# Kernel optimization log

Hardware: AMD Instinct MI355X
Metric: run time of the kernel (lower is better)

## Reference

```python
import jax, jax.numpy as jnp
import numpy as np

N = 50000


def gcn_conv(x, edge_index, W, b):
    # x: [N, F_in], edge_index: [2, E] (row=source j, col=target i)
    n = x.shape[0]
    loops = jnp.arange(n, dtype=edge_index.dtype)
    row = jnp.concatenate([edge_index[0], loops])
    col = jnp.concatenate([edge_index[1], loops])
    # linear transform first (PyG GCNConv)
    xw = x @ W  # [N, F_out]
    # symmetric normalization deg^{-1/2}[row] * deg^{-1/2}[col]
    deg = jax.ops.segment_sum(jnp.ones_like(col, dtype=xw.dtype), col, num_segments=n)
    dis = jnp.where(deg > 0, jax.lax.rsqrt(jnp.maximum(deg, 1e-12)), 0.0)
    norm = dis[row] * dis[col]  # [E+N]
    # gather-scale-scatter: sum_j norm_ij * (W x_j)
    msgs = xw[row] * norm[:, None]
    out = jax.ops.segment_sum(msgs, col, num_segments=n)
    return out + b


def setup_inputs() -> dict:
    key = jax.random.key(0)
    k1, k2, k3, k4, k5 = jax.random.split(key, 5)
    in_dim, hidden_dim, out_dim = 128, 128, 64
    x = jax.random.normal(k1, (N, in_dim), dtype=jnp.float32)
    edge_index = jax.random.randint(k2, (2, 800000), 0, N, dtype=jnp.int64)
    s1 = 1.0 / np.sqrt(in_dim)
    s2 = 1.0 / np.sqrt(hidden_dim)
    W1 = jax.random.uniform(k3, (in_dim, hidden_dim), jnp.float32, -s1, s1)
    b1 = jnp.zeros((hidden_dim,), jnp.float32)
    W2 = jax.random.uniform(k4, (hidden_dim, out_dim), jnp.float32, -s2, s2)
    b2 = jnp.zeros((out_dim,), jnp.float32)
    return {"x": x, "edge_index": edge_index, "W1": W1, "b1": b1, "W2": W2, "b2": b2}


def reference(x, edge_index, W1, b1, W2, b2):
    h = gcn_conv(x, edge_index, W1, b1)
    h = jax.nn.relu(h)
    # dropout(p=0.5, training=False) -> identity (inference reference)
    out = gcn_conv(h, edge_index, W2, b2)
    return out
```

## Files before the change

kernel.cpp:

```cpp
#include <hip/hip_runtime.h>
#include <hip/hip_fp16.h>


typedef _Float16 half8 __attribute__((ext_vector_type(8)));
typedef float floatx4 __attribute__((ext_vector_type(4)));

__global__ void k_count(const int* __restrict__ col, int* __restrict__ deg,
                        int* __restrict__ rank, int E) {
    int e = blockIdx.x * blockDim.x + threadIdx.x;
    if (e < E) rank[e] = atomicAdd(&deg[col[e]], 1);
}

__global__ __launch_bounds__(1024) void k_scan_local(const int* __restrict__ deg,
                                                     int* __restrict__ rowptr,
                                                     int* __restrict__ bsum,
                                                     float* __restrict__ dis, int n) {
    __shared__ int s[1024];
    int b = blockIdx.x, tid = threadIdx.x;
    int i = b * 1024 + tid;
    int v = (i < n) ? deg[i] : 0;
    if (i < n) dis[i] = rsqrtf((float)v + 1.0f);
    s[tid] = v;
    __syncthreads();
    for (int off = 1; off < 1024; off <<= 1) {
        int t = (tid >= off) ? s[tid - off] : 0;
        __syncthreads();
        s[tid] += t;
        __syncthreads();
    }
    if (i < n) rowptr[i + 1] = s[tid];
    if (tid == 1023) bsum[b] = s[1023];
    if (b == 0 && tid == 0) rowptr[0] = 0;
}

__global__ __launch_bounds__(256) void k_scan_fix(int* __restrict__ rowptr,
                                                  const int* __restrict__ bsum, int n) {
    __shared__ int red[256];
    int b = blockIdx.x, tid = threadIdx.x;
    int partial = 0;
    for (int j = tid; j < b; j += 256) partial += bsum[j];
    red[tid] = partial;
    __syncthreads();
    for (int off = 128; off > 0; off >>= 1) {
        if (tid < off) red[tid] += red[tid + off];
        __syncthreads();
    }
    int offv = red[0];
    if (offv == 0) return;
#pragma unroll
    for (int r = 0; r < 4; ++r) {
        int i = b * 1024 + r * 256 + tid;
        if (i < n) rowptr[i + 1] += offv;
    }
}

__global__ void k_fill(const int* __restrict__ row, const int* __restrict__ col,
                       const int* __restrict__ rowptr, const int* __restrict__ rank,
                       int* __restrict__ csr, int E) {
    int e = blockIdx.x * blockDim.x + threadIdx.x;
    if (e < E) csr[rowptr[col[e]] + rank[e]] = row[e];
}

template <int N, typename AT>
__global__ __launch_bounds__(256) void k_gemm_mfma(const AT* __restrict__ X,
                                                   const float* __restrict__ W,
                                                   const float* __restrict__ scale,
                                                   __half* __restrict__ Y, int M) {
    __shared__ __align__(16) __half2 wt[N * 64];
    int tid = threadIdx.x;
    for (int i = tid; i < N * 64; i += 256) {
        int nn = i & (N - 1);
        int k2 = i / N;
        float w0 = W[(size_t)(2 * k2) * N + nn];
        float w1 = W[(size_t)(2 * k2 + 1) * N + nn];
        wt[nn * 64 + ((k2 >> 2) ^ (nn & 15)) * 4 + (k2 & 3)] = __floats2half2_rn(w0, w1);
    }
    __syncthreads();
    int wid = tid >> 6, lane = tid & 63;
    int col = lane & 15, quad = lane >> 4;
    int m_a = blockIdx.x * 64 + wid * 16 + col;
    bool a_ok = m_a < M;
    constexpr int NT = N / 16;
    floatx4 acc[NT] = {};
#pragma unroll
    for (int ks = 0; ks < 4; ++ks) {
        int k = ks * 32 + quad * 8;
        half8 af;
        if constexpr (sizeof(AT) == 4) {
            floatx4 a0 = {0.f, 0.f, 0.f, 0.f}, a1 = {0.f, 0.f, 0.f, 0.f};
            if (a_ok) {
                a0 = *(const floatx4*)&X[(size_t)m_a * 128 + k];
                a1 = *(const floatx4*)&X[(size_t)m_a * 128 + k + 4];
            }
            af = half8{(_Float16)a0[0], (_Float16)a0[1], (_Float16)a0[2], (_Float16)a0[3],
                       (_Float16)a1[0], (_Float16)a1[1], (_Float16)a1[2], (_Float16)a1[3]};
        } else {
            half8 t = {};
            if (a_ok) t = *(const half8*)(const void*)&X[(size_t)m_a * 128 + k];
            af = t;
        }
        int kblk = ks * 4 + quad;
#pragma unroll
        for (int nt = 0; nt < NT; ++nt) {
            int nn = nt * 16 + col;
            half8 bf = *(const half8*)(const void*)&wt[nn * 64 + (kblk ^ (nn & 15)) * 4];
            acc[nt] = __builtin_amdgcn_mfma_f32_16x16x32_f16(af, bf, acc[nt], 0, 0, 0);
        }
    }
    int mbase = blockIdx.x * 64 + wid * 16 + quad * 4;
    float s[4];
#pragma unroll
    for (int r = 0; r < 4; ++r) s[r] = (mbase + r < M) ? scale[mbase + r] : 0.f;
#pragma unroll
    for (int nt = 0; nt < NT; ++nt) {
#pragma unroll
        for (int r = 0; r < 4; ++r) {
            if (mbase + r < M)
                Y[(size_t)(mbase + r) * N + nt * 16 + col] = __float2half(acc[nt][r] * s[r]);
        }
    }
}

__global__ __launch_bounds__(256) void k_agg128(const __half* __restrict__ xw,
                                                const float* __restrict__ dis,
                                                const int* __restrict__ rowptr,
                                                const int* __restrict__ csr,
                                                const float* __restrict__ bias,
                                                __half* __restrict__ out, int n) {
    int tid = threadIdx.x;
    int lane = tid & 63;
    int q = lane >> 4, li = lane & 15;
    int qbase = lane & 48;
    int node = blockIdx.x * 16 + ((tid >> 6) << 2) + q;
    bool ok = node < n;
    float di = 0.f;
    int beg = 0, end = 0;
    if (ok) {
        di = dis[node];
        beg = rowptr[node];
        end = rowptr[node + 1];
    }
    int dg = end - beg;
    int m1 = max(dg, __shfl(dg, lane ^ 16));
    int mx = max(m1, __shfl(m1, lane ^ 32));
    const half8* rows = (const half8*)xw;
    float acc[8] = {};
    if (ok) {
        half8 sf = rows[(size_t)node * 16 + li];
#pragma unroll
        for (int f = 0; f < 8; ++f) acc[f] = (float)sf[f];
    }
    for (int i = 0; i < mx; i += 8) {
        int e = beg + i + (li & 7);
        int myidx = (e < end) ? csr[e] : 0;
        half8 v[8];
#pragma unroll
        for (int j = 0; j < 8; ++j) {
            int s = __shfl(myidx, qbase + j);
            v[j] = rows[(size_t)s * 16 + li];
        }
#pragma unroll
        for (int j = 0; j < 8; ++j) {
            if (beg + i + j < end) {
#pragma unroll
                for (int f = 0; f < 8; ++f) acc[f] += (float)v[j][f];
            }
        }
    }
    if (ok) {
        floatx4 b0 = *(const floatx4*)&bias[li * 8];
        floatx4 b1 = *(const floatx4*)&bias[li * 8 + 4];
        half8 o;
#pragma unroll
        for (int f = 0; f < 4; ++f) o[f] = (_Float16)fmaxf(acc[f] * di + b0[f], 0.f);
#pragma unroll
        for (int f = 0; f < 4; ++f) o[4 + f] = (_Float16)fmaxf(acc[4 + f] * di + b1[f], 0.f);
        ((half8*)out)[(size_t)node * 16 + li] = o;
    }
}

__global__ __launch_bounds__(256) void k_agg64(const __half* __restrict__ xw,
                                               const float* __restrict__ dis,
                                               const int* __restrict__ rowptr,
                                               const int* __restrict__ csr,
                                               const float* __restrict__ bias,
                                               float* __restrict__ out, int n) {
    int tid = threadIdx.x;
    int lane = tid & 63;
    int o8 = lane >> 3, li = lane & 7;
    int obase = lane & 56;
    int node = blockIdx.x * 32 + ((tid >> 6) << 3) + o8;
    bool ok = node < n;
    float di = 0.f;
    int beg = 0, end = 0;
    if (ok) {
        di = dis[node];
        beg = rowptr[node];
        end = rowptr[node + 1];
    }
    int dg = end - beg;
    int m1 = max(dg, __shfl(dg, lane ^ 8));
    int m2 = max(m1, __shfl(m1, lane ^ 16));
    int mx = max(m2, __shfl(m2, lane ^ 32));
    const half8* rows = (const half8*)xw;
    float acc[8] = {};
    if (ok) {
        half8 sf = rows[(size_t)node * 8 + li];
#pragma unroll
        for (int f = 0; f < 8; ++f) acc[f] = (float)sf[f];
    }
    for (int i = 0; i < mx; i += 8) {
        int e = beg + i + li;
        int myidx = (e < end) ? csr[e] : 0;
        half8 v[8];
#pragma unroll
        for (int j = 0; j < 8; ++j) {
            int s = __shfl(myidx, obase + j);
            v[j] = rows[(size_t)s * 8 + li];
        }
#pragma unroll
        for (int j = 0; j < 8; ++j) {
            if (beg + i + j < end) {
#pragma unroll
                for (int f = 0; f < 8; ++f) acc[f] += (float)v[j][f];
            }
        }
    }
    if (ok) {
        floatx4 b0 = *(const floatx4*)&bias[li * 8];
        floatx4 b1 = *(const floatx4*)&bias[li * 8 + 4];
        floatx4 o0, o1;
#pragma unroll
        for (int f = 0; f < 4; ++f) o0[f] = acc[f] * di + b0[f];
#pragma unroll
        for (int f = 0; f < 4; ++f) o1[f] = acc[4 + f] * di + b1[f];
        *(floatx4*)&out[(size_t)node * 64 + li * 8] = o0;
        *(floatx4*)&out[(size_t)node * 64 + li * 8 + 4] = o1;
    }
}

extern "C" void kernel_launch(void* const* d_in, const int* in_sizes, int n_in,
                              void* d_out, int out_size, void* d_ws, size_t ws_size,
                              hipStream_t stream) {
    const float* x  = (const float*)d_in[0];
    const int*   ei = (const int*)d_in[1];
    const float* W1 = (const float*)d_in[2];
    const float* b1 = (const float*)d_in[3];
    const float* W2 = (const float*)d_in[4];
    const float* b2 = (const float*)d_in[5];
    float* out = (float*)d_out;

    const int n = in_sizes[0] / 128;
    const int E = in_sizes[1] / 2;
    const int* row = ei;
    const int* col = ei + E;
    const int NB = (n + 1023) / 1024;
    const int CB = (E + 255) / 256;
    const int GB = (n + 63) / 64;

    char* ws = (char*)d_ws;
    size_t off = 0;
    auto alloc = [&](size_t bytes) -> void* {
        void* p = ws + off;
        off += (bytes + 255) & ~(size_t)255;
        return p;
    };
    int*    deg    = (int*)alloc((size_t)n * 4);
    int*    rowptr = (int*)alloc((size_t)(n + 1) * 4);
    int*    bsum   = (int*)alloc((size_t)NB * 4);
    int*    rank   = (int*)alloc((size_t)E * 4);
    int*    csr    = (int*)alloc((size_t)E * 4);
    float*  dis    = (float*)alloc((size_t)n * 4);
    __half* xw1    = (__half*)alloc((size_t)n * 128 * 2);
    __half* h      = (__half*)alloc((size_t)n * 128 * 2);
    __half* xw2    = (__half*)alloc((size_t)n * 64 * 2);
    (void)ws_size;

    hipMemsetAsync(deg, 0, (size_t)n * 4, stream);
    k_count<<<CB, 256, 0, stream>>>(col, deg, rank, E);
    k_scan_local<<<NB, 1024, 0, stream>>>(deg, rowptr, bsum, dis, n);
    k_scan_fix<<<NB, 256, 0, stream>>>(rowptr, bsum, n);
    k_fill<<<CB, 256, 0, stream>>>(row, col, rowptr, rank, csr, E);

    k_gemm_mfma<128, float><<<GB, 256, 0, stream>>>(x, W1, dis, xw1, n);
    k_agg128<<<(n + 15) / 16, 256, 0, stream>>>(xw1, dis, rowptr, csr, b1, h, n);
    k_gemm_mfma<64, __half><<<GB, 256, 0, stream>>>(h, W2, dis, xw2, n);
    k_agg64<<<(n + 31) / 32, 256, 0, stream>>>(xw2, dis, rowptr, csr, b2, out, n);
}
```

Baseline: 208.2 us.

## Sort nodes by degree bucket to balance aggregation wavefronts

Builds a 64-bucket degree histogram during the scan and a counting-sort permutation of nodes by in-degree, then has both aggregation kernels process nodes in that order. Nodes that share a wavefront then have similar degrees, which cuts the divergence where the loop runs to the maximum degree among grouped nodes. The cost is an extra kernel, atomics, and scattered output and self-row accesses, since permuted node ids are no longer contiguous.

Result: slower. 318.4 us (+52.9%).

```diff
diff --git a/kernel.cpp b/kernel.cpp
--- a/kernel.cpp
+++ b/kernel.cpp
@@ -14,14 +14,18 @@
 __global__ __launch_bounds__(1024) void k_scan_local(const int* __restrict__ deg,
                                                      int* __restrict__ rowptr,
                                                      int* __restrict__ bsum,
-                                                     float* __restrict__ dis, int n) {
+                                                     float* __restrict__ dis,
+                                                     int* __restrict__ hist, int n) {
     __shared__ int s[1024];
+    __shared__ int lh[64];
     int b = blockIdx.x, tid = threadIdx.x;
+    if (tid < 64) lh[tid] = 0;
     int i = b * 1024 + tid;
     int v = (i < n) ? deg[i] : 0;
     if (i < n) dis[i] = rsqrtf((float)v + 1.0f);
     s[tid] = v;
     __syncthreads();
+    if (i < n) atomicAdd(&lh[min(v, 63)], 1);
     for (int off = 1; off < 1024; off <<= 1) {
         int t = (tid >= off) ? s[tid - off] : 0;
         __syncthreads();
@@ -31,6 +35,8 @@
     if (i < n) rowptr[i + 1] = s[tid];
     if (tid == 1023) bsum[b] = s[1023];
     if (b == 0 && tid == 0) rowptr[0] = 0;
+    __syncthreads();
+    if (tid < 64) atomicAdd(&hist[tid], lh[tid]);
 }
 
 __global__ __launch_bounds__(256) void k_scan_fix(int* __restrict__ rowptr,
@@ -59,6 +65,30 @@
                        int* __restrict__ csr, int E) {
     int e = blockIdx.x * blockDim.x + threadIdx.x;
     if (e < E) csr[rowptr[col[e]] + rank[e]] = row[e];
+}
+
+__global__ __launch_bounds__(256) void k_perm(const int* __restrict__ deg,
+                                              const int* __restrict__ hist,
+                                              int* __restrict__ cursor,
+                                              int* __restrict__ perm, int n) {
+    __shared__ int boff[64];
+    int tid = threadIdx.x;
+    if (tid < 64) {
+        int h = hist[tid];
+        int v = h;
+        for (int off = 1; off < 64; off <<= 1) {
+            int t = __shfl_up(v, off);
+            if (tid >= off) v += t;
+        }
+        boff[tid] = v - h;
+    }
+    __syncthreads();
+    int i = blockIdx.x * 256 + tid;
+    if (i < n) {
+        int b = min(deg[i], 63);
+        int pos = boff[b] + atomicAdd(&cursor[b], 1);
+        perm[pos] = i;
+    }
 }
 
 template <int N, typename AT>
@@ -125,14 +155,16 @@
                                                 const float* __restrict__ dis,
                                                 const int* __restrict__ rowptr,
                                                 const int* __restrict__ csr,
+                                                const int* __restrict__ perm,
                                                 const float* __restrict__ bias,
                                                 __half* __restrict__ out, int n) {
     int tid = threadIdx.x;
     int lane = tid & 63;
     int q = lane >> 4, li = lane & 15;
     int qbase = lane & 48;
-    int node = blockIdx.x * 16 + ((tid >> 6) << 2) + q;
-    bool ok = node < n;
+    int gidx = blockIdx.x * 16 + ((tid >> 6) << 2) + q;
+    bool ok = gidx < n;
+    int node = ok ? perm[gidx] : 0;
     float di = 0.f;
     int beg = 0, end = 0;
     if (ok) {
@@ -183,14 +215,16 @@
                                                const float* __restrict__ dis,
                                                const int* __restrict__ rowptr,
                                                const int* __restrict__ csr,
+                                               const int* __restrict__ perm,
                                                const float* __restrict__ bias,
                                                float* __restrict__ out, int n) {
     int tid = threadIdx.x;
     int lane = tid & 63;
     int o8 = lane >> 3, li = lane & 7;
     int obase = lane & 56;
-    int node = blockIdx.x * 32 + ((tid >> 6) << 3) + o8;
-    bool ok = node < n;
+    int gidx = blockIdx.x * 32 + ((tid >> 6) << 3) + o8;
+    bool ok = gidx < n;
+    int node = ok ? perm[gidx] : 0;
     float di = 0.f;
     int beg = 0, end = 0;
     if (ok) {
@@ -265,25 +299,29 @@
         off += (bytes + 255) & ~(size_t)255;
         return p;
     };
-    int*    deg    = (int*)alloc((size_t)n * 4);
+    int*    deg    = (int*)alloc((size_t)(n + 128) * 4);
+    int*    hist   = deg + n;
+    int*    cursor = deg + n + 64;
     int*    rowptr = (int*)alloc((size_t)(n + 1) * 4);
     int*    bsum   = (int*)alloc((size_t)NB * 4);
     int*    rank   = (int*)alloc((size_t)E * 4);
     int*    csr    = (int*)alloc((size_t)E * 4);
+    int*    perm   = (int*)alloc((size_t)n * 4);
     float*  dis    = (float*)alloc((size_t)n * 4);
     __half* xw1    = (__half*)alloc((size_t)n * 128 * 2);
     __half* h      = (__half*)alloc((size_t)n * 128 * 2);
     __half* xw2    = (__half*)alloc((size_t)n * 64 * 2);
     (void)ws_size;
 
-    hipMemsetAsync(deg, 0, (size_t)n * 4, stream);
+    hipMemsetAsync(deg, 0, (size_t)(n + 128) * 4, stream);
     k_count<<<CB, 256, 0, stream>>>(col, deg, rank, E);
-    k_scan_local<<<NB, 1024, 0, stream>>>(deg, rowptr, bsum, dis, n);
+    k_scan_local<<<NB, 1024, 0, stream>>>(deg, rowptr, bsum, dis, hist, n);
     k_scan_fix<<<NB, 256, 0, stream>>>(rowptr, bsum, n);
     k_fill<<<CB, 256, 0, stream>>>(row, col, rowptr, rank, csr, E);
+    k_perm<<<(n + 255) / 256, 256, 0, stream>>>(deg, hist, cursor, perm, n);
 
     k_gemm_mfma<128, float><<<GB, 256, 0, stream>>>(x, W1, dis, xw1, n);
-    k_agg128<<<(n + 15) / 16, 256, 0, stream>>>(xw1, dis, rowptr, csr, b1, h, n);
+    k_agg128<<<(n + 15) / 16, 256, 0, stream>>>(xw1, dis, rowptr, csr, perm, b1, h, n);
     k_gemm_mfma<64, __half><<<GB, 256, 0, stream>>>(h, W2, dis, xw2, n);
-    k_agg64<<<(n + 31) / 32, 256, 0, stream>>>(xw2, dis, rowptr, csr, b2, out, n);
-}
+    k_agg64<<<(n + 31) / 32, 256, 0, stream>>>(xw2, dis, rowptr, csr, perm, b2, out, n);
+}
```

## Use wave-shuffle block scan and fuse scan fixup with first GEMM launch

Applied to the files above, without the earlier changes.

The local prefix scan now uses wavefront shuffles plus a small shared-memory pass over per-wave sums, replacing the shared-memory Hillis-Steele loop that needed many barriers. The scan-fixup kernel and the first GEMM are merged into one launch: the first NB blocks do the fixup and the remaining blocks do GEMM tiles. This removes one kernel launch and lets the two independent jobs run concurrently. The GEMM body moves into a shared device helper, and the fused kernel always allocates the larger shared-memory footprint, even for the fixup blocks.

After: 205.3 us. Within noise of the previous version (-1.4%).

```diff
diff --git a/kernel.cpp b/kernel.cpp
--- a/kernel.cpp
+++ b/kernel.cpp
@@ -15,59 +15,42 @@
                                                      int* __restrict__ rowptr,
                                                      int* __restrict__ bsum,
                                                      float* __restrict__ dis, int n) {
-    __shared__ int s[1024];
+    __shared__ int wsum[16];
     int b = blockIdx.x, tid = threadIdx.x;
+    int lane = tid & 63, w = tid >> 6;
     int i = b * 1024 + tid;
     int v = (i < n) ? deg[i] : 0;
     if (i < n) dis[i] = rsqrtf((float)v + 1.0f);
-    s[tid] = v;
+    int sc = v;
+#pragma unroll
+    for (int off = 1; off < 64; off <<= 1) {
+        int t = __shfl_up(sc, off);
+        if (lane >= off) sc += t;
+    }
+    if (lane == 63) wsum[w] = sc;
     __syncthreads();
-    for (int off = 1; off < 1024; off <<= 1) {
-        int t = (tid >= off) ? s[tid - off] : 0;
-        __syncthreads();
-        s[tid] += t;
-        __syncthreads();
-    }
-    if (i < n) rowptr[i + 1] = s[tid];
-    if (tid == 1023) bsum[b] = s[1023];
+    if (w == 0) {
+        int s = (lane < 16) ? wsum[lane] : 0;
+#pragma unroll
+        for (int off = 1; off < 16; off <<= 1) {
+            int t = __shfl_up(s, off);
+            if (lane >= off) s += t;
+        }
+        if (lane < 16) wsum[lane] = s;
+    }
+    __syncthreads();
+    int incl = sc + ((w > 0) ? wsum[w - 1] : 0);
+    if (i < n) rowptr[i + 1] = incl;
+    if (tid == 1023) bsum[b] = incl;
     if (b == 0 && tid == 0) rowptr[0] = 0;
 }
 
-__global__ __launch_bounds__(256) void k_scan_fix(int* __restrict__ rowptr,
-                                                  const int* __restrict__ bsum, int n) {
-    __shared__ int red[256];
-    int b = blockIdx.x, tid = threadIdx.x;
-    int partial = 0;
-    for (int j = tid; j < b; j += 256) partial += bsum[j];
-    red[tid] = partial;
-    __syncthreads();
-    for (int off = 128; off > 0; off >>= 1) {
-        if (tid < off) red[tid] += red[tid + off];
-        __syncthreads();
-    }
-    int offv = red[0];
-    if (offv == 0) return;
-#pragma unroll
-    for (int r = 0; r < 4; ++r) {
-        int i = b * 1024 + r * 256 + tid;
-        if (i < n) rowptr[i + 1] += offv;
-    }
-}
-
-__global__ void k_fill(const int* __restrict__ row, const int* __restrict__ col,
-                       const int* __restrict__ rowptr, const int* __restrict__ rank,
-                       int* __restrict__ csr, int E) {
-    int e = blockIdx.x * blockDim.x + threadIdx.x;
-    if (e < E) csr[rowptr[col[e]] + rank[e]] = row[e];
-}
-
 template <int N, typename AT>
-__global__ __launch_bounds__(256) void k_gemm_mfma(const AT* __restrict__ X,
-                                                   const float* __restrict__ W,
-                                                   const float* __restrict__ scale,
-                                                   __half* __restrict__ Y, int M) {
-    __shared__ __align__(16) __half2 wt[N * 64];
-    int tid = threadIdx.x;
+__device__ __forceinline__ void gemm_tile(const AT* __restrict__ X,
+                                          const float* __restrict__ W,
+                                          const float* __restrict__ scale,
+                                          __half* __restrict__ Y, int M,
+                                          int m0, __half2* wt, int tid) {
     for (int i = tid; i < N * 64; i += 256) {
         int nn = i & (N - 1);
         int k2 = i / N;
@@ -78,7 +61,7 @@
     __syncthreads();
     int wid = tid >> 6, lane = tid & 63;
     int col = lane & 15, quad = lane >> 4;
-    int m_a = blockIdx.x * 64 + wid * 16 + col;
+    int m_a = m0 + wid * 16 + col;
     bool a_ok = m_a < M;
     constexpr int NT = N / 16;
     floatx4 acc[NT] = {};
@@ -107,7 +90,7 @@
             acc[nt] = __builtin_amdgcn_mfma_f32_16x16x32_f16(af, bf, acc[nt], 0, 0, 0);
         }
     }
-    int mbase = blockIdx.x * 64 + wid * 16 + quad * 4;
+    int mbase = m0 + wid * 16 + quad * 4;
     float s[4];
 #pragma unroll
     for (int r = 0; r < 4; ++r) s[r] = (mbase + r < M) ? scale[mbase + r] : 0.f;
@@ -119,6 +102,51 @@
                 Y[(size_t)(mbase + r) * N + nt * 16 + col] = __float2half(acc[nt][r] * s[r]);
         }
     }
+}
+
+__global__ __launch_bounds__(256) void k_fix_gemm1(int* __restrict__ rowptr,
+                                                   const int* __restrict__ bsum, int n,
+                                                   const float* __restrict__ X,
+                                                   const float* __restrict__ W,
+                                                   const float* __restrict__ scale,
+                                                   __half* __restrict__ Y, int M, int FB) {
+    __shared__ __align__(16) __half2 wt[128 * 64];
+    int b = blockIdx.x, tid = threadIdx.x;
+    if (b < FB) {
+        int* red = (int*)wt;
+        int partial = 0;
+        for (int j = tid; j < b; j += 256) partial += bsum[j];
+        red[tid] = partial;
+        __syncthreads();
+        for (int off = 128; off > 0; off >>= 1) {
+            if (tid < off) red[tid] += red[tid + off];
+            __syncthreads();
+        }
+        int offv = red[0];
+        if (offv == 0) return;
+#pragma unroll
+        for (int r = 0; r < 4; ++r) {
+            int i = b * 1024 + r * 256 + tid;
+            if (i < n) rowptr[i + 1] += offv;
+        }
+        return;
+    }
+    gemm_tile<128, float>(X, W, scale, Y, M, (b - FB) * 64, wt, tid);
+}
+
+__global__ __launch_bounds__(256) void k_gemm2(const __half* __restrict__ X,
+                                               const float* __restrict__ W,
+                                               const float* __restrict__ scale,
+                                               __half* __restrict__ Y, int M) {
+    __shared__ __align__(16) __half2 wt[64 * 64];
+    gemm_tile<64, __half>(X, W, scale, Y, M, blockIdx.x * 64, wt, threadIdx.x);
+}
+
+__global__ void k_fill(const int* __restrict__ row, const int* __restrict__ col,
+                       const int* __restrict__ rowptr, const int* __restrict__ rank,
+                       int* __restrict__ csr, int E) {
+    int e = blockIdx.x * blockDim.x + threadIdx.x;
+    if (e < E) csr[rowptr[col[e]] + rank[e]] = row[e];
 }
 
 __global__ __launch_bounds__(256) void k_agg128(const __half* __restrict__ xw,
@@ -279,11 +307,10 @@
     hipMemsetAsync(deg, 0, (size_t)n * 4, stream);
     k_count<<<CB, 256, 0, stream>>>(col, deg, rank, E);
     k_scan_local<<<NB, 1024, 0, stream>>>(deg, rowptr, bsum, dis, n);
-    k_scan_fix<<<NB, 256, 0, stream>>>(rowptr, bsum, n);
+    k_fix_gemm1<<<NB + GB, 256, 0, stream>>>(rowptr, bsum, n, x, W1, dis, xw1, n, NB);
     k_fill<<<CB, 256, 0, stream>>>(row, col, rowptr, rank, csr, E);
 
-    k_gemm_mfma<128, float><<<GB, 256, 0, stream>>>(x, W1, dis, xw1, n);
     k_agg128<<<(n + 15) / 16, 256, 0, stream>>>(xw1, dis, rowptr, csr, b1, h, n);
-    k_gemm_mfma<64, __half><<<GB, 256, 0, stream>>>(h, W2, dis, xw2, n);
+    k_gemm2<<<GB, 256, 0, stream>>>(h, W2, dis, xw2, n);
     k_agg64<<<(n + 31) / 32, 256, 0, stream>>>(xw2, dis, rowptr, csr, b2, out, n);
 }
```
